# Kernel optimization log

Hardware: AMD Instinct MI355X
Metric: run time of the kernel (lower is better)

## Reference

```python
import jax, jax.numpy as jnp
import numpy as np


def _lstm_step(x, h, c, Wih, Whh, bih, bhh):
    # PyTorch LSTMCell gate order: i, f, g, o
    g = x @ Wih.T + bih + h @ Whh.T + bhh
    i, f, gg, o = jnp.split(g, 4, axis=1)
    c = jax.nn.sigmoid(f) * c + jax.nn.sigmoid(i) * jnp.tanh(gg)
    h = jax.nn.sigmoid(o) * jnp.tanh(c)
    return h, c


def _canvas2seq(canvas):
    # Valid objects (row-sum >= 0) compacted to the front, rest padded with -1.
    mask = canvas.sum(axis=2) >= 0                       # [B, 25]
    order = jnp.argsort(jnp.where(mask, 0, 1), axis=1, stable=True)
    gathered = jnp.take_along_axis(canvas, order[:, :, None], axis=1)
    smask = jnp.take_along_axis(mask, order, axis=1)
    return jnp.where(smask[:, :, None], gathered, jnp.float32(-1.0))


def _canvas_encode(canvas, Wobj, bobj, ce_Wih, ce_Whh, ce_bih, ce_bhh):
    seq = _canvas2seq(canvas)                            # [B, 25, 4]
    x = seq @ Wobj.T + bobj                              # [B, 25, 64]
    B = x.shape[0]
    h = jnp.zeros((B, 64), x.dtype)
    c = jnp.zeros((B, 64), x.dtype)

    def step(carry, xt):
        h, c = carry
        h, c = _lstm_step(xt, h, c, ce_Wih, ce_Whh, ce_bih, ce_bhh)
        return (h, c), None

    (h, _), _ = jax.lax.scan(step, (h, c), jnp.swapaxes(x, 0, 1))
    return h


def setup_inputs() -> dict:
    key = jax.random.key(0)
    ks = jax.random.split(key, 16)
    B, T, V = 256, 65, 10000
    IN, H = 64, 128
    s = 0.05
    inp = {}
    inp["inst"] = jax.random.randint(ks[0], (B, T), 0, V)
    inp["prev_canvas"] = jax.random.uniform(ks[1], (B, 25, 4), dtype=jnp.float32)
    inp["final_canvas"] = jax.random.uniform(ks[2], (B, 25, 4), dtype=jnp.float32)
    inp["target_obj"] = jax.random.normal(ks[3], (B, 4), dtype=jnp.float32)
    inp["embed_W"] = jax.random.normal(ks[4], (V + 1, IN), dtype=jnp.float32) * s
    inp["Wih"] = jax.random.normal(ks[5], (4 * H, IN), dtype=jnp.float32) * s
    inp["Whh"] = jax.random.normal(ks[6], (4 * H, H), dtype=jnp.float32) * s
    inp["bih"] = jnp.zeros((4 * H,), jnp.float32)
    inp["bhh"] = jnp.zeros((4 * H,), jnp.float32)
    inp["Wout"] = jax.random.normal(ks[7], (V + 1, H), dtype=jnp.float32) * s
    inp["bout"] = jnp.zeros((V + 1,), jnp.float32)
    inp["Wtgt"] = jax.random.normal(ks[8], (IN, 4), dtype=jnp.float32) * s
    inp["btgt"] = jnp.zeros((IN,), jnp.float32)
    inp["Wobj"] = jax.random.normal(ks[9], (64, 4), dtype=jnp.float32) * s
    inp["bobj"] = jnp.zeros((64,), jnp.float32)
    inp["ce_Wih"] = jax.random.normal(ks[10], (256, 64), dtype=jnp.float32) * s
    inp["ce_Whh"] = jax.random.normal(ks[11], (256, 64), dtype=jnp.float32) * s
    inp["ce_bih"] = jnp.zeros((256,), jnp.float32)
    inp["ce_bhh"] = jnp.zeros((256,), jnp.float32)
    return inp


def reference(inst, prev_canvas, final_canvas, target_obj,
              embed_W, Wih, Whh, bih, bhh, Wout, bout,
              Wtgt, btgt, Wobj, bobj, ce_Wih, ce_Whh, ce_bih, ce_bhh):
    B, H = inst.shape[0], 128
    tgt_emb = target_obj @ Wtgt.T + btgt                 # [B, 64]
    enc = (_canvas_encode(prev_canvas, Wobj, bobj, ce_Wih, ce_Whh, ce_bih, ce_bhh)
           + _canvas_encode(final_canvas, Wobj, bobj, ce_Wih, ce_Whh, ce_bih, ce_bhh))
    h = jnp.zeros((B, H), jnp.float32)
    c = jnp.zeros((B, H), jnp.float32)
    h, c = _lstm_step(enc, h, c, Wih, Whh, bih, bhh)
    h, c = _lstm_step(tgt_emb, h, c, Wih, Whh, bih, bhh)

    tokens = inst[:, :-1].T                              # [T-1, B]

    def step(carry, it):
        h, c = carry
        xt = embed_W[it]                                 # [B, 64]
        h, c = _lstm_step(xt, h, c, Wih, Whh, bih, bhh)
        lp = jax.nn.log_softmax(h @ Wout.T + bout, axis=1)
        return (h, c), lp

    _, lps = jax.lax.scan(step, (h, c), tokens)          # [T-1, B, V+1]
    return jnp.swapaxes(lps, 0, 1)                       # [B, T-1, V+1]
```

## Files before the change

kernel.cpp:

```cpp
#include <hip/hip_runtime.h>
#include <stdint.h>

typedef __attribute__((ext_vector_type(4))) float f32x4;
typedef __attribute__((ext_vector_type(8))) short s16x8;
typedef __attribute__((ext_vector_type(8))) unsigned short us8;

__device__ __forceinline__ float bf2f(unsigned short u){
  union { unsigned int i; float f; } v; v.i = ((unsigned int)u) << 16; return v.f;
}
__device__ __forceinline__ unsigned short f2bf(float f){
  union { float f; unsigned int i; } v; v.f = f;
  unsigned int r = v.i + 0x7FFFu + ((v.i >> 16) & 1u);
  return (unsigned short)(r >> 16);
}
__device__ __forceinline__ float sigm(float x){ return 1.0f / (1.0f + __expf(-x)); }

#define NA (10112*128)
#define NB 10112
#define ND 512
#define NE (256*64)

__global__ void k_prep(const float* __restrict__ Wout, const float* __restrict__ bout,
                       const float* __restrict__ bih,  const float* __restrict__ bhh,
                       const float* __restrict__ tobj, const float* __restrict__ Wtgt,
                       const float* __restrict__ btgt,
                       unsigned short* __restrict__ WoutP, float* __restrict__ boutP,
                       float* __restrict__ bsum, float* __restrict__ tgt)
{
  int tid = blockIdx.x * 256 + threadIdx.x;
  if (tid < NA){
    int vv = tid >> 7, k = tid & 127;
    float val = (vv < 10001) ? Wout[vv*128 + k] : 0.0f;
    WoutP[tid] = f2bf(val);
  } else if (tid < NA+NB){
    int vv = tid - NA;
    boutP[vv] = (vv < 10001) ? bout[vv] : -1e30f;
  } else if (tid < NA+NB+ND){
    int g = tid - NA - NB;
    bsum[g] = bih[g] + bhh[g];
  } else if (tid < NA+NB+ND+NE){
    int i = tid - NA - NB - ND; int b = i >> 6, j = i & 63;
    const float* to = tobj + b*4; const float* wt = Wtgt + j*4;
    tgt[i] = btgt[j] + to[0]*wt[0] + to[1]*wt[1] + to[2]*wt[2] + to[3]*wt[3];
  }
}

__global__ __launch_bounds__(256) void k_canvas(
    const float* __restrict__ prevC, const float* __restrict__ finC,
    const float* __restrict__ Wobj,  const float* __restrict__ bobj,
    const float* __restrict__ ceWih, const float* __restrict__ ceWhh,
    const float* __restrict__ cebih, const float* __restrict__ cebhh,
    float* __restrict__ encP, float* __restrict__ encF)
{
  __shared__ unsigned short wih[256*64] __attribute__((aligned(16)));
  __shared__ unsigned short whh[256*64] __attribute__((aligned(16)));
  __shared__ float seq[25*4];
  __shared__ float xb[64] __attribute__((aligned(16)));
  __shared__ float hb[2][64] __attribute__((aligned(16)));
  __shared__ float gates[256];
  __shared__ float wobj_s[256];
  __shared__ float bobj_s[64];
  __shared__ float bsum_ce[256];

  int tid = threadIdx.x;
  int b = blockIdx.x & 255;
  int which = blockIdx.x >> 8;
  const float* canvas = (which ? finC : prevC) + b*100;

  for (int i = tid; i < 2048; i += 256){
    int g = i >> 3, k8 = i & 7;
    const float* s1 = ceWih + g*64 + k8*8;
    const float* s2 = ceWhh + g*64 + k8*8;
    us8 v1, v2;
    #pragma unroll
    for (int j = 0; j < 8; j++){ v1[j] = f2bf(s1[j]); v2[j] = f2bf(s2[j]); }
    int slot = ((k8 ^ (g & 7)) * 8);
    *reinterpret_cast<us8*>(&wih[g*64 + slot]) = v1;
    *reinterpret_cast<us8*>(&whh[g*64 + slot]) = v2;
  }
  wobj_s[tid] = Wobj[tid];
  if (tid < 64) bobj_s[tid] = bobj[tid];
  bsum_ce[tid] = cebih[tid] + cebhh[tid];
  if (tid < 64) hb[0][tid] = 0.0f;
  if (tid == 0){
    int pos = 0;
    for (int i = 0; i < 25; i++){
      float a0=canvas[i*4+0], a1=canvas[i*4+1], a2=canvas[i*4+2], a3=canvas[i*4+3];
      if (a0+a1+a2+a3 >= 0.0f){
        seq[pos*4+0]=a0; seq[pos*4+1]=a1; seq[pos*4+2]=a2; seq[pos*4+3]=a3; pos++;
      }
    }
    for (; pos < 25; pos++){
      seq[pos*4+0]=-1.0f; seq[pos*4+1]=-1.0f; seq[pos*4+2]=-1.0f; seq[pos*4+3]=-1.0f;
    }
  }
  __syncthreads();

  float creg = 0.0f;
  int cur = 0;
  const float4* x4 = (const float4*)xb;

  for (int t = 0; t < 25; t++){
    if (tid < 64){
      float a = bobj_s[tid];
      a += wobj_s[tid*4+0]*seq[t*4+0] + wobj_s[tid*4+1]*seq[t*4+1]
         + wobj_s[tid*4+2]*seq[t*4+2] + wobj_s[tid*4+3]*seq[t*4+3];
      xb[tid] = a;
    }
    __syncthreads();
    float acc = bsum_ce[tid];
    const float4* h4 = (const float4*)hb[cur];
    int rowoff = tid*64;
    int sw = tid & 7;
    #pragma unroll
    for (int k8 = 0; k8 < 8; k8++){
      int slot = ((k8 ^ sw) * 8);
      us8 w1 = *reinterpret_cast<const us8*>(&wih[rowoff + slot]);
      us8 w2 = *reinterpret_cast<const us8*>(&whh[rowoff + slot]);
      float4 xa = x4[2*k8], xc = x4[2*k8+1];
      float4 ha = h4[2*k8], hc = h4[2*k8+1];
      acc += bf2f(w1[0])*xa.x + bf2f(w1[1])*xa.y + bf2f(w1[2])*xa.z + bf2f(w1[3])*xa.w;
      acc += bf2f(w1[4])*xc.x + bf2f(w1[5])*xc.y + bf2f(w1[6])*xc.z + bf2f(w1[7])*xc.w;
      acc += bf2f(w2[0])*ha.x + bf2f(w2[1])*ha.y + bf2f(w2[2])*ha.z + bf2f(w2[3])*ha.w;
      acc += bf2f(w2[4])*hc.x + bf2f(w2[5])*hc.y + bf2f(w2[6])*hc.z + bf2f(w2[7])*hc.w;
    }
    gates[tid] = acc;
    __syncthreads();
    if (tid < 64){
      float i_ = sigm(gates[tid]);
      float f_ = sigm(gates[64+tid]);
      float g_ = tanhf(gates[128+tid]);
      float o_ = sigm(gates[192+tid]);
      creg = f_*creg + i_*g_;
      hb[cur^1][tid] = o_ * tanhf(creg);
    }
    __syncthreads();
    cur ^= 1;
  }
  if (tid < 64){
    (which ? encF : encP)[b*64 + tid] = hb[cur][tid];
  }
}

__global__ __launch_bounds__(512, 2) void k_rec(
    const float* __restrict__ Whh, const float* __restrict__ Wih,
    const float* __restrict__ bsum, const int* __restrict__ inst,
    const float* __restrict__ embW, const float* __restrict__ tgt,
    const float* __restrict__ encP, const float* __restrict__ encF,
    unsigned short* __restrict__ Hout)
{
  int b = blockIdx.x;
  int g = threadIdx.x;
  __shared__ float xb[2][64] __attribute__((aligned(16)));
  __shared__ float hb[2][128] __attribute__((aligned(16)));
  __shared__ float gates[512];

  float wreg[128];
  float ureg[64];
  {
    const float4* wrow = (const float4*)(Whh + g*128);
    #pragma unroll
    for (int k4 = 0; k4 < 32; k4++){
      float4 w = wrow[k4];
      wreg[4*k4+0]=w.x; wreg[4*k4+1]=w.y; wreg[4*k4+2]=w.z; wreg[4*k4+3]=w.w;
    }
    const float4* urow = (const float4*)(Wih + g*64);
    #pragma unroll
    for (int k4 = 0; k4 < 16; k4++){
      float4 w = urow[k4];
      ureg[4*k4+0]=w.x; ureg[4*k4+1]=w.y; ureg[4*k4+2]=w.z; ureg[4*k4+3]=w.w;
    }
  }
  float bz = bsum[g];
  float creg = 0.0f;
  if (g < 128) hb[0][g] = 0.0f;
  if (g < 64)  xb[0][g] = encP[b*64+g] + encF[b*64+g];
  int cur = 0;
  __syncthreads();

  for (int s = 0; s < 66; s++){
    float a0 = bz, a1 = 0.0f, a2 = 0.0f, a3 = 0.0f;
    const float4* h4 = (const float4*)hb[cur];
    const float4* x4 = (const float4*)xb[cur];
    #pragma unroll
    for (int k4 = 0; k4 < 32; k4 += 4){
      float4 h0 = h4[k4], h1 = h4[k4+1], h2 = h4[k4+2], h3 = h4[k4+3];
      a0 += wreg[4*k4+0]*h0.x + wreg[4*k4+1]*h0.y + wreg[4*k4+2]*h0.z + wreg[4*k4+3]*h0.w;
      a1 += wreg[4*k4+4]*h1.x + wreg[4*k4+5]*h1.y + wreg[4*k4+6]*h1.z + wreg[4*k4+7]*h1.w;
      a2 += wreg[4*k4+8]*h2.x + wreg[4*k4+9]*h2.y + wreg[4*k4+10]*h2.z + wreg[4*k4+11]*h2.w;
      a3 += wreg[4*k4+12]*h3.x + wreg[4*k4+13]*h3.y + wreg[4*k4+14]*h3.z + wreg[4*k4+15]*h3.w;
    }
    #pragma unroll
    for (int k4 = 0; k4 < 16; k4 += 4){
      float4 x0 = x4[k4], x1 = x4[k4+1], x2 = x4[k4+2], x3 = x4[k4+3];
      a0 += ureg[4*k4+0]*x0.x + ureg[4*k4+1]*x0.y + ureg[4*k4+2]*x0.z + ureg[4*k4+3]*x0.w;
      a1 += ureg[4*k4+4]*x1.x + ureg[4*k4+5]*x1.y + ureg[4*k4+6]*x1.z + ureg[4*k4+7]*x1.w;
      a2 += ureg[4*k4+8]*x2.x + ureg[4*k4+9]*x2.y + ureg[4*k4+10]*x2.z + ureg[4*k4+11]*x2.w;
      a3 += ureg[4*k4+12]*x3.x + ureg[4*k4+13]*x3.y + ureg[4*k4+14]*x3.z + ureg[4*k4+15]*x3.w;
    }
    gates[g] = (a0 + a1) + (a2 + a3);
    __syncthreads();
    if (g < 128){
      float i_ = sigm(gates[g]);
      float f_ = sigm(gates[128+g]);
      float g_ = tanhf(gates[256+g]);
      float o_ = sigm(gates[384+g]);
      creg = f_*creg + i_*g_;
      float h = o_ * tanhf(creg);
      hb[cur^1][g] = h;
      if (s >= 2) Hout[((s-2)*256 + b)*128 + g] = f2bf(h);
    } else if (g < 192 && s < 65){
      int l = g - 128;
      float v;
      if (s + 1 == 1) v = tgt[b*64 + l];
      else { int tok = inst[b*65 + (s - 1)]; v = embW[tok*64 + l]; }
      xb[cur^1][l] = v;
    }
    __syncthreads();
    cur ^= 1;
  }
}

__global__ __launch_bounds__(512, 4) void k_out(
    const unsigned short* __restrict__ Hout, const unsigned short* __restrict__ WoutP,
    const float* __restrict__ boutP, float* __restrict__ out)
{
  int blk = blockIdx.x;
  int t = blk >> 3;
  int b0 = (blk & 7) * 32;
  int r0 = t*256 + b0;
  int tid = threadIdx.x;
  int w = tid >> 6;
  int l = tid & 63;
  int lm = l & 15;
  int lq = l >> 4;
  int kof = lq * 8;

  __shared__ float rs_l[8][32];
  __shared__ float lse_l[32];
  __shared__ float stage[2][32][132] __attribute__((aligned(16)));

  s16x8 af0[4], af1[4];
  {
    const s16x8* ap0 = (const s16x8*)(Hout + (size_t)(r0 + lm)*128 + kof);
    const s16x8* ap1 = (const s16x8*)(Hout + (size_t)(r0 + 16 + lm)*128 + kof);
    #pragma unroll
    for (int kk = 0; kk < 4; kk++){ af0[kk] = ap0[kk*4]; af1[kk] = ap1[kk*4]; }
  }

  s16x8 bA[4], bB[4];
#define LOADB(dst, tl) { \
    const s16x8* bp_ = (const s16x8*)(WoutP + (size_t)((tl)*16 + lm)*128 + kof); \
    dst[0] = bp_[0]; dst[1] = bp_[4]; dst[2] = bp_[8]; dst[3] = bp_[12]; }

  float rs0[4] = {0,0,0,0}, rs1[4] = {0,0,0,0};
#define P1COMP(buf, tl) { \
    f32x4 a0_ = {0,0,0,0}, a1_ = {0,0,0,0}; \
    _Pragma("unroll") \
    for (int kk = 0; kk < 4; kk++){ \
      a0_ = __builtin_amdgcn_mfma_f32_16x16x32_bf16(af0[kk], buf[kk], a0_, 0, 0, 0); \
      a1_ = __builtin_amdgcn_mfma_f32_16x16x32_bf16(af1[kk], buf[kk], a1_, 0, 0, 0); } \
    float bo_ = boutP[(tl)*16 + lm]; \
    _Pragma("unroll") \
    for (int i = 0; i < 4; i++){ rs0[i] += __expf(a0_[i] + bo_); rs1[i] += __expf(a1_[i] + bo_); } }

  {
    int tl = w;
    LOADB(bA, tl);
    for (int it = 0; it < 39; it++){
      LOADB(bB, tl + 8);
      P1COMP(bA, tl);
      LOADB(bA, tl + 16);
      P1COMP(bB, tl + 8);
      tl += 16;
    }
    P1COMP(bA, tl);
  }

  #pragma unroll
  for (int i = 0; i < 4; i++){
    float s0 = rs0[i], s1 = rs1[i];
    s0 += __shfl_xor(s0, 1); s0 += __shfl_xor(s0, 2); s0 += __shfl_xor(s0, 4); s0 += __shfl_xor(s0, 8);
    s1 += __shfl_xor(s1, 1); s1 += __shfl_xor(s1, 2); s1 += __shfl_xor(s1, 4); s1 += __shfl_xor(s1, 8);
    rs0[i] = s0; rs1[i] = s1;
  }
  if (lm == 0){
    #pragma unroll
    for (int i = 0; i < 4; i++){
      rs_l[w][lq*4 + i] = rs0[i];
      rs_l[w][16 + lq*4 + i] = rs1[i];
    }
  }
  __syncthreads();
  if (tid < 32){
    float s = rs_l[0][tid] + rs_l[1][tid] + rs_l[2][tid] + rs_l[3][tid]
            + rs_l[4][tid] + rs_l[5][tid] + rs_l[6][tid] + rs_l[7][tid];
    lse_l[tid] = logf(s);
  }
  __syncthreads();
  float ml0[4], ml1[4];
  #pragma unroll
  for (int i = 0; i < 4; i++){ ml0[i] = lse_l[lq*4 + i]; ml1[i] = lse_l[16 + lq*4 + i]; }

  int col = w*16 + lm;
#define P2COMP(buf, c) { \
    f32x4 a0_ = {0,0,0,0}, a1_ = {0,0,0,0}; \
    _Pragma("unroll") \
    for (int kk = 0; kk < 4; kk++){ \
      a0_ = __builtin_amdgcn_mfma_f32_16x16x32_bf16(af0[kk], buf[kk], a0_, 0, 0, 0); \
      a1_ = __builtin_amdgcn_mfma_f32_16x16x32_bf16(af1[kk], buf[kk], a1_, 0, 0, 0); } \
    float bo_ = boutP[((c)*8 + w)*16 + lm]; \
    float (*sb_)[132] = stage[(c) & 1]; \
    _Pragma("unroll") \
    for (int i = 0; i < 4; i++){ \
      sb_[lq*4 + i][col]      = a0_[i] + bo_ - ml0[i]; \
      sb_[16 + lq*4 + i][col] = a1_[i] + bo_ - ml1[i]; } }

#define BAR() { asm volatile("s_waitcnt lgkmcnt(0)" ::: "memory"); __builtin_amdgcn_s_barrier(); }

#define WPHASE(c) { \
    float (*sb_)[132] = stage[(c) & 1]; \
    int vbase_ = (c)*128; \
    if ((c) < 78){ \
      _Pragma("unroll") \
      for (int j = 0; j < 8; j++){ \
        int e_ = j*512 + tid; int row_ = e_ >> 7; int cc_ = e_ & 127; \
        size_t oidx_ = (size_t)((b0 + row_)*64 + t)*10001u + (unsigned)(vbase_ + cc_); \
        __builtin_nontemporal_store(sb_[row_][cc_], &out[oidx_]); } \
    } else { \
      _Pragma("unroll") \
      for (int j = 0; j < 8; j++){ \
        int e_ = j*512 + tid; int row_ = e_ >> 7; int cc_ = e_ & 127; \
        int v_ = vbase_ + cc_; \
        if (v_ < 10001){ \
          size_t oidx_ = (size_t)((b0 + row_)*64 + t)*10001u + (unsigned)v_; \
          __builtin_nontemporal_store(sb_[row_][cc_], &out[oidx_]); } } } }

  LOADB(bA, w);
  for (int cp = 0; cp < 39; cp++){
    int c = cp*2;
    LOADB(bB, (c + 1)*8 + w);
    P2COMP(bA, c);
    BAR();
    WPHASE(c);
    LOADB(bA, (c + 2)*8 + w);
    P2COMP(bB, c + 1);
    BAR();
    WPHASE(c + 1);
  }
  P2COMP(bA, 78);
  BAR();
  WPHASE(78);
}

extern "C" void kernel_launch(void* const* d_in, const int* in_sizes, int n_in,
                              void* d_out, int out_size, void* d_ws, size_t ws_size,
                              hipStream_t stream)
{
  (void)in_sizes; (void)n_in; (void)out_size; (void)ws_size;
  const int*   inst    = (const int*)  d_in[0];
  const float* prevC   = (const float*)d_in[1];
  const float* finC    = (const float*)d_in[2];
  const float* tobj    = (const float*)d_in[3];
  const float* embW    = (const float*)d_in[4];
  const float* Wih     = (const float*)d_in[5];
  const float* Whh     = (const float*)d_in[6];
  const float* bih     = (const float*)d_in[7];
  const float* bhh     = (const float*)d_in[8];
  const float* Wout    = (const float*)d_in[9];
  const float* bout    = (const float*)d_in[10];
  const float* Wtgt    = (const float*)d_in[11];
  const float* btgt    = (const float*)d_in[12];
  const float* Wobj    = (const float*)d_in[13];
  const float* bobj    = (const float*)d_in[14];
  const float* ceWih   = (const float*)d_in[15];
  const float* ceWhh   = (const float*)d_in[16];
  const float* cebih   = (const float*)d_in[17];
  const float* cebhh   = (const float*)d_in[18];

  char* ws = (char*)d_ws;
  unsigned short* WoutP = (unsigned short*)(ws + 0);
  float* boutP = (float*)(ws + 2588672);
  float* bsum  = (float*)(ws + 2629120);
  float* tgt   = (float*)(ws + 2631168);
  float* encP  = (float*)(ws + 2696704);
  float* encF  = (float*)(ws + 2762240);
  unsigned short* Hout = (unsigned short*)(ws + 2827776);
  float* out = (float*)d_out;

  k_prep  <<<5162, 256, 0, stream>>>(Wout, bout, bih, bhh, tobj, Wtgt, btgt,
                                     WoutP, boutP, bsum, tgt);
  k_canvas<<<512, 256, 0, stream>>>(prevC, finC, Wobj, bobj, ceWih, ceWhh,
                                    cebih, cebhh, encP, encF);
  k_rec   <<<256, 512, 0, stream>>>(Whh, Wih, bsum, inst, embW, tgt, encP, encF, Hout);
  k_out   <<<512, 512, 0, stream>>>(Hout, WoutP, boutP, out);
}
```

Before: 592.7 us.

## Widen output tiles to 256 vocab columns and prepack canvas LSTM weights once

The output projection kernel now computes two 128-column vocab tiles per phase, staging 32x256 rows in dynamic shared memory and storing 256 contiguous floats per row. This halves the number of barrier/store phases, lengthens contiguous write runs to the large output tensor, and pads Wout to 10240 rows. Separately, the bf16 conversion and swizzling of the canvas LSTM weights moves into the prep kernel, so each of the 512 canvas blocks copies prepacked data instead of converting fp32 itself. In exchange it uses more registers and shared memory (about 66KB per block), which may lower occupancy under the launch bound of 4 blocks.

```diff
diff --git a/kernel.cpp b/kernel.cpp
--- a/kernel.cpp
+++ b/kernel.cpp
@@ -15,17 +15,20 @@
 }
 __device__ __forceinline__ float sigm(float x){ return 1.0f / (1.0f + __expf(-x)); }
 
-#define NA (10112*128)
-#define NB 10112
+#define NA (10240*128)
+#define NB 10240
 #define ND 512
 #define NE (256*64)
+#define NF 32768
 
 __global__ void k_prep(const float* __restrict__ Wout, const float* __restrict__ bout,
                        const float* __restrict__ bih,  const float* __restrict__ bhh,
                        const float* __restrict__ tobj, const float* __restrict__ Wtgt,
                        const float* __restrict__ btgt,
+                       const float* __restrict__ ceWih, const float* __restrict__ ceWhh,
                        unsigned short* __restrict__ WoutP, float* __restrict__ boutP,
-                       float* __restrict__ bsum, float* __restrict__ tgt)
+                       float* __restrict__ bsum, float* __restrict__ tgt,
+                       unsigned short* __restrict__ cePack)
 {
   int tid = blockIdx.x * 256 + threadIdx.x;
   if (tid < NA){
@@ -42,13 +45,22 @@
     int i = tid - NA - NB - ND; int b = i >> 6, j = i & 63;
     const float* to = tobj + b*4; const float* wt = Wtgt + j*4;
     tgt[i] = btgt[j] + to[0]*wt[0] + to[1]*wt[1] + to[2]*wt[2] + to[3]*wt[3];
+  } else if (tid < NA+NB+ND+NE+NF){
+    int i = tid - NA - NB - ND - NE;
+    int half = i >> 14;
+    int r = (i >> 6) & 255;
+    int k = i & 63;
+    int k8 = k >> 3;
+    int slot = ((k8 ^ (r & 7)) << 3) | (k & 7);
+    const float* src = half ? ceWhh : ceWih;
+    cePack[half*16384 + r*64 + slot] = f2bf(src[r*64 + k]);
   }
 }
 
 __global__ __launch_bounds__(256) void k_canvas(
     const float* __restrict__ prevC, const float* __restrict__ finC,
     const float* __restrict__ Wobj,  const float* __restrict__ bobj,
-    const float* __restrict__ ceWih, const float* __restrict__ ceWhh,
+    const unsigned short* __restrict__ cePack,
     const float* __restrict__ cebih, const float* __restrict__ cebhh,
     float* __restrict__ encP, float* __restrict__ encF)
 {
@@ -67,16 +79,14 @@
   int which = blockIdx.x >> 8;
   const float* canvas = (which ? finC : prevC) + b*100;
 
-  for (int i = tid; i < 2048; i += 256){
-    int g = i >> 3, k8 = i & 7;
-    const float* s1 = ceWih + g*64 + k8*8;
-    const float* s2 = ceWhh + g*64 + k8*8;
-    us8 v1, v2;
-    #pragma unroll
-    for (int j = 0; j < 8; j++){ v1[j] = f2bf(s1[j]); v2[j] = f2bf(s2[j]); }
-    int slot = ((k8 ^ (g & 7)) * 8);
-    *reinterpret_cast<us8*>(&wih[g*64 + slot]) = v1;
-    *reinterpret_cast<us8*>(&whh[g*64 + slot]) = v2;
+  {
+    const us8* cp = (const us8*)cePack;
+    us8* wl = (us8*)wih;
+    us8* hl = (us8*)whh;
+    for (int i = tid; i < 2048; i += 256){
+      wl[i] = cp[i];
+      hl[i] = cp[2048 + i];
+    }
   }
   wobj_s[tid] = Wobj[tid];
   if (tid < 64) bobj_s[tid] = bobj[tid];
@@ -221,10 +231,16 @@
   }
 }
 
+#define ROWSTR ((size_t)64*10001)
+
 __global__ __launch_bounds__(512, 4) void k_out(
     const unsigned short* __restrict__ Hout, const unsigned short* __restrict__ WoutP,
     const float* __restrict__ boutP, float* __restrict__ out)
 {
+  extern __shared__ float stage[];
+  __shared__ float rs_l[8][32];
+  __shared__ float lse_l[32];
+
   int blk = blockIdx.x;
   int t = blk >> 3;
   int b0 = (blk & 7) * 32;
@@ -235,10 +251,7 @@
   int lm = l & 15;
   int lq = l >> 4;
   int kof = lq * 8;
-
-  __shared__ float rs_l[8][32];
-  __shared__ float lse_l[32];
-  __shared__ float stage[2][32][132] __attribute__((aligned(16)));
+  size_t obase = ((size_t)b0*64 + (size_t)t)*10001u;
 
   s16x8 af0[4], af1[4];
   {
@@ -248,7 +261,7 @@
     for (int kk = 0; kk < 4; kk++){ af0[kk] = ap0[kk*4]; af1[kk] = ap1[kk*4]; }
   }
 
-  s16x8 bA[4], bB[4];
+  s16x8 c0A[4], c0B[4], c1A[4], c1B[4];
 #define LOADB(dst, tl) { \
     const s16x8* bp_ = (const s16x8*)(WoutP + (size_t)((tl)*16 + lm)*128 + kof); \
     dst[0] = bp_[0]; dst[1] = bp_[4]; dst[2] = bp_[8]; dst[3] = bp_[12]; }
@@ -266,15 +279,17 @@
 
   {
     int tl = w;
-    LOADB(bA, tl);
+    LOADB(c0A, tl);
     for (int it = 0; it < 39; it++){
-      LOADB(bB, tl + 8);
-      P1COMP(bA, tl);
-      LOADB(bA, tl + 16);
-      P1COMP(bB, tl + 8);
+      LOADB(c0B, tl + 8);
+      P1COMP(c0A, tl);
+      LOADB(c0A, tl + 16);
+      P1COMP(c0B, tl + 8);
       tl += 16;
     }
-    P1COMP(bA, tl);
+    LOADB(c0B, tl + 8);
+    P1COMP(c0A, tl);
+    P1COMP(c0B, tl + 8);
   }
 
   #pragma unroll
@@ -302,55 +317,54 @@
   #pragma unroll
   for (int i = 0; i < 4; i++){ ml0[i] = lse_l[lq*4 + i]; ml1[i] = lse_l[16 + lq*4 + i]; }
 
-  int col = w*16 + lm;
-#define P2COMP(buf, c) { \
-    f32x4 a0_ = {0,0,0,0}, a1_ = {0,0,0,0}; \
+  int colA = w*16 + lm;
+#define P2COMP2(bufA, bufB, c) { \
+    f32x4 p0_ = {0,0,0,0}, p1_ = {0,0,0,0}, q0_ = {0,0,0,0}, q1_ = {0,0,0,0}; \
     _Pragma("unroll") \
     for (int kk = 0; kk < 4; kk++){ \
-      a0_ = __builtin_amdgcn_mfma_f32_16x16x32_bf16(af0[kk], buf[kk], a0_, 0, 0, 0); \
-      a1_ = __builtin_amdgcn_mfma_f32_16x16x32_bf16(af1[kk], buf[kk], a1_, 0, 0, 0); } \
-    float bo_ = boutP[((c)*8 + w)*16 + lm]; \
-    float (*sb_)[132] = stage[(c) & 1]; \
+      p0_ = __builtin_amdgcn_mfma_f32_16x16x32_bf16(af0[kk], bufA[kk], p0_, 0, 0, 0); \
+      p1_ = __builtin_amdgcn_mfma_f32_16x16x32_bf16(af1[kk], bufA[kk], p1_, 0, 0, 0); \
+      q0_ = __builtin_amdgcn_mfma_f32_16x16x32_bf16(af0[kk], bufB[kk], q0_, 0, 0, 0); \
+      q1_ = __builtin_amdgcn_mfma_f32_16x16x32_bf16(af1[kk], bufB[kk], q1_, 0, 0, 0); } \
+    float boA_ = boutP[((c)*16 + w)*16 + lm]; \
+    float boB_ = boutP[((c)*16 + 8 + w)*16 + lm]; \
+    float* sb_ = stage + ((c)&1)*(32*258); \
     _Pragma("unroll") \
     for (int i = 0; i < 4; i++){ \
-      sb_[lq*4 + i][col]      = a0_[i] + bo_ - ml0[i]; \
-      sb_[16 + lq*4 + i][col] = a1_[i] + bo_ - ml1[i]; } }
+      sb_[(lq*4+i)*258 + colA]        = p0_[i] + boA_ - ml0[i]; \
+      sb_[(16+lq*4+i)*258 + colA]     = p1_[i] + boA_ - ml1[i]; \
+      sb_[(lq*4+i)*258 + 128 + colA]  = q0_[i] + boB_ - ml0[i]; \
+      sb_[(16+lq*4+i)*258 + 128 + colA] = q1_[i] + boB_ - ml1[i]; } }
 
 #define BAR() { asm volatile("s_waitcnt lgkmcnt(0)" ::: "memory"); __builtin_amdgcn_s_barrier(); }
 
 #define WPHASE(c) { \
-    float (*sb_)[132] = stage[(c) & 1]; \
-    int vbase_ = (c)*128; \
-    if ((c) < 78){ \
+    const float* sb_ = stage + ((c)&1)*(32*258); \
+    int vbase_ = (c)*256; \
+    if ((c) < 39){ \
       _Pragma("unroll") \
-      for (int j = 0; j < 8; j++){ \
-        int e_ = j*512 + tid; int row_ = e_ >> 7; int cc_ = e_ & 127; \
-        size_t oidx_ = (size_t)((b0 + row_)*64 + t)*10001u + (unsigned)(vbase_ + cc_); \
-        __builtin_nontemporal_store(sb_[row_][cc_], &out[oidx_]); } \
+      for (int j = 0; j < 16; j++){ \
+        int e_ = j*512 + tid; int row_ = e_ >> 8; int cc_ = e_ & 255; \
+        __builtin_nontemporal_store(sb_[row_*258 + cc_], &out[obase + (size_t)row_*ROWSTR + (unsigned)(vbase_ + cc_)]); } \
     } else { \
       _Pragma("unroll") \
-      for (int j = 0; j < 8; j++){ \
-        int e_ = j*512 + tid; int row_ = e_ >> 7; int cc_ = e_ & 127; \
-        int v_ = vbase_ + cc_; \
-        if (v_ < 10001){ \
-          size_t oidx_ = (size_t)((b0 + row_)*64 + t)*10001u + (unsigned)v_; \
-          __builtin_nontemporal_store(sb_[row_][cc_], &out[oidx_]); } } } }
-
-  LOADB(bA, w);
-  for (int cp = 0; cp < 39; cp++){
+      for (int j = 0; j < 16; j++){ \
+        int e_ = j*512 + tid; int row_ = e_ >> 8; int cc_ = e_ & 255; \
+        if (vbase_ + cc_ < 10001) \
+          __builtin_nontemporal_store(sb_[row_*258 + cc_], &out[obase + (size_t)row_*ROWSTR + (unsigned)(vbase_ + cc_)]); } } }
+
+  LOADB(c0A, w); LOADB(c0B, 8 + w);
+  for (int cp = 0; cp < 20; cp++){
     int c = cp*2;
-    LOADB(bB, (c + 1)*8 + w);
-    P2COMP(bA, c);
+    P2COMP2(c0A, c0B, c);
+    LOADB(c1A, (c+1)*16 + w); LOADB(c1B, (c+1)*16 + 8 + w);
     BAR();
     WPHASE(c);
-    LOADB(bA, (c + 2)*8 + w);
-    P2COMP(bB, c + 1);
+    P2COMP2(c1A, c1B, c+1);
+    if (c + 2 < 40){ LOADB(c0A, (c+2)*16 + w); LOADB(c0B, (c+2)*16 + 8 + w); }
     BAR();
-    WPHASE(c + 1);
-  }
-  P2COMP(bA, 78);
-  BAR();
-  WPHASE(78);
+    WPHASE(c+1);
+  }
 }
 
 extern "C" void kernel_launch(void* const* d_in, const int* in_sizes, int n_in,
@@ -380,18 +394,22 @@
 
   char* ws = (char*)d_ws;
   unsigned short* WoutP = (unsigned short*)(ws + 0);
-  float* boutP = (float*)(ws + 2588672);
-  float* bsum  = (float*)(ws + 2629120);
-  float* tgt   = (float*)(ws + 2631168);
-  float* encP  = (float*)(ws + 2696704);
-  float* encF  = (float*)(ws + 2762240);
-  unsigned short* Hout = (unsigned short*)(ws + 2827776);
+  float* boutP = (float*)(ws + 2621440);
+  float* bsum  = (float*)(ws + 2662400);
+  float* tgt   = (float*)(ws + 2664448);
+  float* encP  = (float*)(ws + 2729984);
+  float* encF  = (float*)(ws + 2795520);
+  unsigned short* Hout = (unsigned short*)(ws + 2861056);
+  unsigned short* cePack = (unsigned short*)(ws + 7055360);
   float* out = (float*)d_out;
 
-  k_prep  <<<5162, 256, 0, stream>>>(Wout, bout, bih, bhh, tobj, Wtgt, btgt,
-                                     WoutP, boutP, bsum, tgt);
-  k_canvas<<<512, 256, 0, stream>>>(prevC, finC, Wobj, bobj, ceWih, ceWhh,
+  hipFuncSetAttribute((const void*)k_out,
+                      hipFuncAttributeMaxDynamicSharedMemorySize, 66048);
+
+  k_prep  <<<5354, 256, 0, stream>>>(Wout, bout, bih, bhh, tobj, Wtgt, btgt,
+                                     ceWih, ceWhh, WoutP, boutP, bsum, tgt, cePack);
+  k_canvas<<<512, 256, 0, stream>>>(prevC, finC, Wobj, bobj, cePack,
                                     cebih, cebhh, encP, encF);
   k_rec   <<<256, 512, 0, stream>>>(Whh, Wih, bsum, inst, embW, tgt, encP, encF, Hout);
-  k_out   <<<512, 512, 0, stream>>>(Hout, WoutP, boutP, out);
-}
+  k_out   <<<512, 512, 66048, stream>>>(Hout, WoutP, boutP, out);
+}
```

After: 630.1 us. +6.3%, slower.
